# Performance work log

Hardware: AMD Instinct MI355X
Metric: run time of the kernel (lower is better)

The kernel has to match this reference:

```python
import jax, jax.numpy as jnp
import numpy as np

D_M = 1024
NUM_TOK = 4096


def setup_inputs() -> dict:
    key = jax.random.key(0)
    ks = jax.random.split(key, 7)
    mk = lambda k, shp: jax.random.normal(k, shp, dtype=jnp.float32) * 0.02
    return {
        "X": jax.random.normal(ks[0], (D_M, NUM_TOK), dtype=jnp.float32),
        "W_Q": mk(ks[1], (D_M, D_M)),
        "W_K": mk(ks[2], (D_M, D_M)),
        "W_V": mk(ks[3], (D_M, D_M)),
        "W_O": mk(ks[4], (D_M, D_M)),
        "mlp_in": mk(ks[5], (D_M, D_M)),
        "mlp_out": mk(ks[6], (D_M, D_M)),
    }


def reference(X, W_Q, W_K, W_V, W_O, mlp_in, mlp_out):
    # X: [d_m, num_tok]; module transposes to tokens-major [N, d]
    Xt = X.T  # [N, d]
    N = Xt.shape[0]
    Q = Xt @ W_Q  # [N, d]
    K = Xt @ W_K  # [N, d]
    scores = Q @ K.T  # [N, N] -- NOTE: no 1/sqrt(d) scaling, as in the original
    causal = jnp.tril(jnp.ones((N, N), dtype=bool))  # keep lower triangle incl. diag
    scores = jnp.where(causal, scores, -jnp.inf)
    A = jax.nn.softmax(scores, axis=-1)  # [N, N]
    # original applies W_V then W_O to X BEFORE the attention mix
    RH = (Xt @ W_V) @ W_O  # [N, d]
    Xt = Xt + A @ RH  # residual + attention
    h = jax.nn.relu(Xt @ mlp_in)  # [N, d] (hidden dim == d_m in original)
    Xt = Xt + h @ mlp_out  # residual + MLP
    return Xt.T  # back to [d_m, num_tok]
```

## Files before the change

kernel.cpp:

```cpp
#include <hip/hip_runtime.h>
#include <stdint.h>
#include <stddef.h>

using f16 = _Float16;
typedef __attribute__((ext_vector_type(8))) _Float16 f16x8;
typedef __attribute__((ext_vector_type(4))) float f32x4;

__device__ __forceinline__ void async_copy16(const f16* g, f16* l) {
    __builtin_amdgcn_global_load_lds(
        (const __attribute__((address_space(1))) void*)g,
        (__attribute__((address_space(3))) void*)l, 16, 0, 0);
}

__global__ __launch_bounds__(256)
void transpose_x(const float* __restrict__ in, float* __restrict__ outF,
                 f16* __restrict__ outH, int R, int C) {
    __shared__ float tile[32][33];
    const int tx = threadIdx.x & 31, ty = threadIdx.x >> 5;
    const int c0 = blockIdx.x * 32, r0 = blockIdx.y * 32;
#pragma unroll
    for (int j = 0; j < 4; j++)
        tile[ty + j * 8][tx] = in[(size_t)(r0 + ty + j * 8) * C + c0 + tx];
    __syncthreads();
#pragma unroll
    for (int j = 0; j < 4; j++) {
        float v = tile[tx][ty + j * 8];
        size_t idx = (size_t)(c0 + ty + j * 8) * R + r0 + tx;
        outF[idx] = v;
        outH[idx] = (f16)v;
    }
}

__global__ __launch_bounds__(256)
void prep_w(const float* __restrict__ w0, const float* __restrict__ w1,
            const float* __restrict__ w2, const float* __restrict__ w3,
            const float* __restrict__ w4, const float* __restrict__ w5,
            f16* o0, f16* o1, f16* o2, f16* o3, f16* o4, f16* o5, int D) {
    const int z = blockIdx.z;
    const float* in = z == 0 ? w0 : z == 1 ? w1 : z == 2 ? w2 : z == 3 ? w3 : z == 4 ? w4 : w5;
    f16* out = z == 0 ? o0 : z == 1 ? o1 : z == 2 ? o2 : z == 3 ? o3 : z == 4 ? o4 : o5;
    const int tx = threadIdx.x & 31, ty = threadIdx.x >> 5;
    const int c0 = blockIdx.x * 32, r0 = blockIdx.y * 32;
    if (z < 3) {
#pragma unroll
        for (int j = 0; j < 4; j++) {
            size_t idx = (size_t)(r0 + ty + j * 8) * D + c0 + tx;
            out[idx] = (f16)in[idx];
        }
    } else {
        __shared__ float tile[32][33];
#pragma unroll
        for (int j = 0; j < 4; j++)
            tile[ty + j * 8][tx] = in[(size_t)(r0 + ty + j * 8) * D + c0 + tx];
        __syncthreads();
#pragma unroll
        for (int j = 0; j < 4; j++)
            out[(size_t)(c0 + ty + j * 8) * D + r0 + tx] = (f16)tile[tx][ty + j * 8];
    }
}

__global__ __launch_bounds__(256)
void softmax_causal_inplace(float* __restrict__ S, int N) {
    const int row = blockIdx.x;
    const int len = row + 1;
    const int lim = ((row >> 7) + 1) << 7;
    float* s = S + (size_t)row * N;
    f16* a = (f16*)s;
    __shared__ float red[256];
    const int t = threadIdx.x;

    float v[16];
    float mx = -1e30f;
#pragma unroll
    for (int j = 0; j < 16; j++) {
        int c = t + j * 256;
        if (c < len) { v[j] = s[c]; mx = fmaxf(mx, v[j]); }
    }
    red[t] = mx; __syncthreads();
    for (int o = 128; o > 0; o >>= 1) { if (t < o) red[t] = fmaxf(red[t], red[t + o]); __syncthreads(); }
    mx = red[0]; __syncthreads();

    float sum = 0.f;
#pragma unroll
    for (int j = 0; j < 16; j++) {
        int c = t + j * 256;
        if (c < len) sum += __expf(v[j] - mx);
    }
    red[t] = sum; __syncthreads();
    for (int o = 128; o > 0; o >>= 1) { if (t < o) red[t] += red[t + o]; __syncthreads(); }
    const float inv = 1.0f / red[0];
#pragma unroll
    for (int j = 0; j < 16; j++) {
        int c = t + j * 256;
        if (c < lim) a[c] = (f16)((c < len) ? __expf(v[j] - mx) * inv : 0.0f);
    }
}

template <int MODE>
__device__ __forceinline__ void body64(
    f16* lA, f16* lB, const f16* __restrict__ A, const f16* __restrict__ B,
    float* __restrict__ Cf, f16* __restrict__ Ch, const float* __restrict__ resid,
    int m0, int n0, int M, int N, int K, int lda, int Keff) {
    const int t = threadIdx.x;
    const int lane = t & 63, wave = t >> 6;
    const int wm = (wave >> 1) * 32, wn = (wave & 1) * 32;
    const int lm = lane & 15, lq = lane >> 4;
    const int sr = t >> 2, sc = (t & 3) * 8;

    f32x4 acc[2][2] = {};

    for (int k0 = 0; k0 < Keff; k0 += 128) {
#pragma unroll
        for (int r = 0; r < 4; r++)
            async_copy16(A + (size_t)(m0 + sr) * lda + k0 + r * 32 + sc,
                         lA + r * 2048 + t * 8);
#pragma unroll
        for (int r = 0; r < 4; r++)
            async_copy16(B + (size_t)(n0 + sr) * K + k0 + r * 32 + sc,
                         lB + r * 2048 + t * 8);
        __syncthreads();

#pragma unroll
        for (int kk = 0; kk < 4; kk++) {
            f16x8 af[2], bf[2];
#pragma unroll
            for (int i = 0; i < 2; i++)
                af[i] = *(const f16x8*)&lA[kk * 2048 + (wm + i * 16 + lm) * 32 + lq * 8];
#pragma unroll
            for (int j = 0; j < 2; j++)
                bf[j] = *(const f16x8*)&lB[kk * 2048 + (wn + j * 16 + lm) * 32 + lq * 8];
#pragma unroll
            for (int i = 0; i < 2; i++)
#pragma unroll
                for (int j = 0; j < 2; j++)
                    acc[i][j] = __builtin_amdgcn_mfma_f32_16x16x32_f16(
                        af[i], bf[j], acc[i][j], 0, 0, 0);
        }
        __syncthreads();
    }

#pragma unroll
    for (int i = 0; i < 2; i++) {
        const int row = m0 + wm + i * 16 + lq * 4;
#pragma unroll
        for (int j = 0; j < 2; j++) {
            const int col = n0 + wn + j * 16 + lm;
            f32x4 v = acc[i][j];
#pragma unroll
            for (int r = 0; r < 4; r++) {
                if (MODE == 0) {
                    Ch[(size_t)(row + r) * N + col] = (f16)v[r];
                } else if (MODE == 1) {
                    Cf[(size_t)(row + r) * N + col] = v[r];
                } else if (MODE == 2) {
                    float o = v[r] + resid[(size_t)(row + r) * N + col];
                    Cf[(size_t)(row + r) * N + col] = o;
                    Ch[(size_t)(row + r) * N + col] = (f16)o;
                } else if (MODE == 3) {
                    Ch[(size_t)(row + r) * N + col] = (f16)fmaxf(v[r], 0.0f);
                } else {
                    float o = v[r] + resid[(size_t)(row + r) * N + col];
                    Cf[(size_t)col * M + (row + r)] = o;
                }
            }
        }
    }
}

__global__ __launch_bounds__(256, 4)
void tiny_pair(const f16* Wkh, const f16* Wqh, f16* GT,
               const f16* Wot, const f16* Wvh, f16* HT) {
    __shared__ alignas(16) f16 smem[16384];
    const int b = blockIdx.x;
    if (b < 256)
        body64<0>(smem, smem + 8192, Wkh, Wqh, nullptr, GT, nullptr,
                  (b >> 4) * 64, (b & 15) * 64, 1024, 1024, 1024, 1024, 1024);
    else {
        const int r = b - 256;
        body64<0>(smem, smem + 8192, Wot, Wvh, nullptr, HT, nullptr,
                  (r >> 4) * 64, (r & 15) * 64, 1024, 1024, 1024, 1024, 1024);
    }
}

__global__ __launch_bounds__(256, 4)
void mid_pair(const f16* Xth, const f16* GT, f16* Qp,
              const f16* HT, f16* RHt) {
    __shared__ alignas(16) f16 smem[16384];
    const int x = blockIdx.x & 7;
    int s = blockIdx.x >> 3;
    if (s < 128) {
        const int m = x + 8 * (s >> 4), n = s & 15;
        body64<0>(smem, smem + 8192, Xth, GT, nullptr, Qp, nullptr,
                  m * 64, n * 64, 4096, 1024, 1024, 1024, 1024);
    } else {
        s -= 128;
        const int n = x + 8 * (s >> 4), m = s & 15;
        body64<0>(smem, smem + 8192, HT, Xth, nullptr, RHt, nullptr,
                  m * 64, n * 64, 1024, 4096, 1024, 1024, 1024);
    }
}

__global__ __launch_bounds__(256, 4)
void scores_tri(const f16* Qp, const f16* Xth, float* S) {
    __shared__ alignas(16) f16 smem[16384];
    const int x = blockIdx.x & 7;
    int s = blockIdx.x >> 3;
    int m = 0, n = 0;
#pragma unroll
    for (int q = 7; q >= 0; q--) {
        const int mm = 8 * q + ((q & 1) ? 7 - x : x);
        if (s < mm + 1) { m = mm; n = s; break; }
        s -= mm + 1;
    }
    body64<1>(smem, smem + 8192, Qp, Xth, S, nullptr, nullptr,
              m * 64, n * 64, 4096, 4096, 1024, 1024, 1024);
}

template <int MODE, bool CAUSAL_K>
__global__ __launch_bounds__(256, 4)
void gemm_narrow(const f16* __restrict__ A, const f16* __restrict__ B,
                 float* __restrict__ Cf, f16* __restrict__ Ch,
                 const float* __restrict__ resid, int M, int N, int K, int lda) {
    __shared__ alignas(16) f16 smem[16384];
    const int x = blockIdx.x & 7, s = blockIdx.x >> 3;
    const int q = 7 - (s >> 4), n = s & 15;
    const int m = CAUSAL_K ? (8 * q + ((q & 1) ? 7 - x : x)) : (x + 8 * q);
    const int m0 = m * 64, n0 = n * 64;
    int Keff = K;
    if (CAUSAL_K) {
        Keff = ((m0 + 64 + 127) >> 7) << 7;
        if (Keff > K) Keff = K;
    }
    body64<MODE>(smem, smem + 8192, A, B, Cf, Ch, resid,
                 m0, n0, M, N, K, lda, Keff);
}

extern "C" void kernel_launch(void* const* d_in, const int* in_sizes, int n_in,
                              void* d_out, int out_size, void* d_ws, size_t ws_size,
                              hipStream_t stream) {
    const int D = 1024, NT = 4096;
    const float* X = (const float*)d_in[0];
    const float* W[6] = {(const float*)d_in[1], (const float*)d_in[2],
                         (const float*)d_in[3], (const float*)d_in[4],
                         (const float*)d_in[5], (const float*)d_in[6]};
    char* ws = (char*)d_ws;
    auto MB = [](size_t x) { return x << 20; };

    float* Xtf  = (float*)(ws + MB(0));
    f16*   Xth  = (f16*)(ws + MB(16));
    f16*   Wqh  = (f16*)(ws + MB(24));
    f16*   Wkh  = (f16*)(ws + MB(26));
    f16*   Wvh  = (f16*)(ws + MB(28));
    f16*   Wot  = (f16*)(ws + MB(30));
    f16*   W4t  = (f16*)(ws + MB(32));
    f16*   W5t  = (f16*)(ws + MB(34));
    f16*   GT   = (f16*)(ws + MB(36));
    f16*   HT   = (f16*)(ws + MB(38));
    f16*   Qp   = (f16*)(ws + MB(40));
    float* S    = (float*)(ws + MB(48));
    f16*   RHt  = (f16*)(ws + MB(112));
    float* Y1f  = (float*)(ws + MB(120));
    f16*   Y1h  = (f16*)(ws + MB(136));
    f16*   hb   = (f16*)(ws + MB(40));
    float* outF = (float*)d_out;

    transpose_x<<<dim3(NT / 32, D / 32), 256, 0, stream>>>(X, Xtf, Xth, D, NT);
    prep_w<<<dim3(D / 32, D / 32, 6), 256, 0, stream>>>(
        W[0], W[1], W[2], W[3], W[4], W[5], Wqh, Wkh, Wvh, Wot, W4t, W5t, D);

    tiny_pair<<<512, 256, 0, stream>>>(Wkh, Wqh, GT, Wot, Wvh, HT);

    mid_pair<<<2048, 256, 0, stream>>>(Xth, GT, Qp, HT, RHt);

    scores_tri<<<2080, 256, 0, stream>>>(Qp, Xth, S);

    softmax_causal_inplace<<<NT, 256, 0, stream>>>(S, NT);
    f16* Ab = (f16*)S;

    gemm_narrow<2, true><<<1024, 256, 0, stream>>>(
        Ab, RHt, Y1f, Y1h, Xtf, NT, D, NT, 2 * NT);

    gemm_narrow<3, false><<<1024, 256, 0, stream>>>(
        Y1h, W4t, nullptr, hb, nullptr, NT, D, D, D);

    gemm_narrow<4, false><<<1024, 256, 0, stream>>>(
        hb, W5t, outF, nullptr, Y1f, NT, D, D, D);
}
```

Measured before the change: 258.9 us.

## Store attention scores in fp16 and vectorize softmax; merge prep kernels

The scores GEMM now writes fp16 logits instead of fp32. Softmax reads and writes them in place with 8-wide vector accesses, and the attention GEMM reads the matrix with a normal row stride. This halves the memory traffic for the large N×N score matrix. The two input-prep kernels are merged into one launch to save a launch. Storing unscaled logits in fp16 risks overflow or precision loss, because scores are not divided by sqrt(d).

```diff
diff --git a/kernel.cpp b/kernel.cpp
--- a/kernel.cpp
+++ b/kernel.cpp
@@ -13,34 +13,36 @@
 }
 
 __global__ __launch_bounds__(256)
-void transpose_x(const float* __restrict__ in, float* __restrict__ outF,
-                 f16* __restrict__ outH, int R, int C) {
+void prep_all(const float* __restrict__ X, float* __restrict__ Xtf,
+              f16* __restrict__ Xth,
+              const float* __restrict__ w0, const float* __restrict__ w1,
+              const float* __restrict__ w2, const float* __restrict__ w3,
+              const float* __restrict__ w4, const float* __restrict__ w5,
+              f16* o0, f16* o1, f16* o2, f16* o3, f16* o4, f16* o5,
+              int D, int NT) {
     __shared__ float tile[32][33];
     const int tx = threadIdx.x & 31, ty = threadIdx.x >> 5;
-    const int c0 = blockIdx.x * 32, r0 = blockIdx.y * 32;
-#pragma unroll
-    for (int j = 0; j < 4; j++)
-        tile[ty + j * 8][tx] = in[(size_t)(r0 + ty + j * 8) * C + c0 + tx];
-    __syncthreads();
-#pragma unroll
-    for (int j = 0; j < 4; j++) {
-        float v = tile[tx][ty + j * 8];
-        size_t idx = (size_t)(c0 + ty + j * 8) * R + r0 + tx;
-        outF[idx] = v;
-        outH[idx] = (f16)v;
-    }
-}
-
-__global__ __launch_bounds__(256)
-void prep_w(const float* __restrict__ w0, const float* __restrict__ w1,
-            const float* __restrict__ w2, const float* __restrict__ w3,
-            const float* __restrict__ w4, const float* __restrict__ w5,
-            f16* o0, f16* o1, f16* o2, f16* o3, f16* o4, f16* o5, int D) {
-    const int z = blockIdx.z;
+    int b = blockIdx.x;
+    if (b < 4096) {
+        const int c0 = (b & 127) * 32, r0 = (b >> 7) * 32;
+#pragma unroll
+        for (int j = 0; j < 4; j++)
+            tile[ty + j * 8][tx] = X[(size_t)(r0 + ty + j * 8) * NT + c0 + tx];
+        __syncthreads();
+#pragma unroll
+        for (int j = 0; j < 4; j++) {
+            float v = tile[tx][ty + j * 8];
+            size_t idx = (size_t)(c0 + ty + j * 8) * D + r0 + tx;
+            Xtf[idx] = v;
+            Xth[idx] = (f16)v;
+        }
+        return;
+    }
+    b -= 4096;
+    const int z = b >> 10, r = b & 1023;
     const float* in = z == 0 ? w0 : z == 1 ? w1 : z == 2 ? w2 : z == 3 ? w3 : z == 4 ? w4 : w5;
     f16* out = z == 0 ? o0 : z == 1 ? o1 : z == 2 ? o2 : z == 3 ? o3 : z == 4 ? o4 : o5;
-    const int tx = threadIdx.x & 31, ty = threadIdx.x >> 5;
-    const int c0 = blockIdx.x * 32, r0 = blockIdx.y * 32;
+    const int c0 = (r & 31) * 32, r0 = (r >> 5) * 32;
     if (z < 3) {
 #pragma unroll
         for (int j = 0; j < 4; j++) {
@@ -48,7 +50,6 @@
             out[idx] = (f16)in[idx];
         }
     } else {
-        __shared__ float tile[32][33];
 #pragma unroll
         for (int j = 0; j < 4; j++)
             tile[ty + j * 8][tx] = in[(size_t)(r0 + ty + j * 8) * D + c0 + tx];
@@ -60,21 +61,30 @@
 }
 
 __global__ __launch_bounds__(256)
-void softmax_causal_inplace(float* __restrict__ S, int N) {
-    const int row = blockIdx.x;
-    const int len = row + 1;
+void softmax_rows(f16* __restrict__ A, int N) {
+    const int row = blockIdx.x, len = row + 1;
     const int lim = ((row >> 7) + 1) << 7;
-    float* s = S + (size_t)row * N;
-    f16* a = (f16*)s;
+    f16* a = A + (size_t)row * N;
     __shared__ float red[256];
     const int t = threadIdx.x;
 
     float v[16];
     float mx = -1e30f;
 #pragma unroll
-    for (int j = 0; j < 16; j++) {
-        int c = t + j * 256;
-        if (c < len) { v[j] = s[c]; mx = fmaxf(mx, v[j]); }
+    for (int j = 0; j < 2; j++) {
+        const int c = (t + j * 256) * 8;
+        if (c < len) {
+            f16x8 x = *(const f16x8*)(a + c);
+#pragma unroll
+            for (int e = 0; e < 8; e++) {
+                float f = (c + e < len) ? (float)x[e] : -1e30f;
+                v[j * 8 + e] = f;
+                mx = fmaxf(mx, f);
+            }
+        } else {
+#pragma unroll
+            for (int e = 0; e < 8; e++) v[j * 8 + e] = -1e30f;
+        }
     }
     red[t] = mx; __syncthreads();
     for (int o = 128; o > 0; o >>= 1) { if (t < o) red[t] = fmaxf(red[t], red[t + o]); __syncthreads(); }
@@ -82,17 +92,23 @@
 
     float sum = 0.f;
 #pragma unroll
-    for (int j = 0; j < 16; j++) {
-        int c = t + j * 256;
-        if (c < len) sum += __expf(v[j] - mx);
+    for (int k = 0; k < 16; k++) {
+        float e = (v[k] > -1e29f) ? __expf(v[k] - mx) : 0.0f;
+        v[k] = e;
+        sum += e;
     }
     red[t] = sum; __syncthreads();
     for (int o = 128; o > 0; o >>= 1) { if (t < o) red[t] += red[t + o]; __syncthreads(); }
     const float inv = 1.0f / red[0];
 #pragma unroll
-    for (int j = 0; j < 16; j++) {
-        int c = t + j * 256;
-        if (c < lim) a[c] = (f16)((c < len) ? __expf(v[j] - mx) * inv : 0.0f);
+    for (int j = 0; j < 2; j++) {
+        const int c = (t + j * 256) * 8;
+        if (c < lim) {
+            f16x8 o8;
+#pragma unroll
+            for (int e = 0; e < 8; e++) o8[e] = (f16)(v[j * 8 + e] * inv);
+            *(f16x8*)(a + c) = o8;
+        }
     }
 }
 
@@ -201,7 +217,7 @@
 }
 
 __global__ __launch_bounds__(256, 4)
-void scores_tri(const f16* Qp, const f16* Xth, float* S) {
+void scores_tri(const f16* Qp, const f16* Xth, f16* Af) {
     __shared__ alignas(16) f16 smem[16384];
     const int x = blockIdx.x & 7;
     int s = blockIdx.x >> 3;
@@ -212,7 +228,7 @@
         if (s < mm + 1) { m = mm; n = s; break; }
         s -= mm + 1;
     }
-    body64<1>(smem, smem + 8192, Qp, Xth, S, nullptr, nullptr,
+    body64<0>(smem, smem + 8192, Qp, Xth, nullptr, Af, nullptr,
               m * 64, n * 64, 4096, 4096, 1024, 1024, 1024);
 }
 
@@ -257,28 +273,27 @@
     f16*   GT   = (f16*)(ws + MB(36));
     f16*   HT   = (f16*)(ws + MB(38));
     f16*   Qp   = (f16*)(ws + MB(40));
-    float* S    = (float*)(ws + MB(48));
-    f16*   RHt  = (f16*)(ws + MB(112));
-    float* Y1f  = (float*)(ws + MB(120));
-    f16*   Y1h  = (f16*)(ws + MB(136));
+    f16*   Af   = (f16*)(ws + MB(48));
+    f16*   RHt  = (f16*)(ws + MB(80));
+    float* Y1f  = (float*)(ws + MB(88));
+    f16*   Y1h  = (f16*)(ws + MB(104));
     f16*   hb   = (f16*)(ws + MB(40));
     float* outF = (float*)d_out;
 
-    transpose_x<<<dim3(NT / 32, D / 32), 256, 0, stream>>>(X, Xtf, Xth, D, NT);
-    prep_w<<<dim3(D / 32, D / 32, 6), 256, 0, stream>>>(
-        W[0], W[1], W[2], W[3], W[4], W[5], Wqh, Wkh, Wvh, Wot, W4t, W5t, D);
+    prep_all<<<10240, 256, 0, stream>>>(X, Xtf, Xth, W[0], W[1], W[2], W[3],
+                                        W[4], W[5], Wqh, Wkh, Wvh, Wot, W4t,
+                                        W5t, D, NT);
 
     tiny_pair<<<512, 256, 0, stream>>>(Wkh, Wqh, GT, Wot, Wvh, HT);
 
     mid_pair<<<2048, 256, 0, stream>>>(Xth, GT, Qp, HT, RHt);
 
-    scores_tri<<<2080, 256, 0, stream>>>(Qp, Xth, S);
-
-    softmax_causal_inplace<<<NT, 256, 0, stream>>>(S, NT);
-    f16* Ab = (f16*)S;
+    scores_tri<<<2080, 256, 0, stream>>>(Qp, Xth, Af);
+
+    softmax_rows<<<NT, 256, 0, stream>>>(Af, NT);
 
     gemm_narrow<2, true><<<1024, 256, 0, stream>>>(
-        Ab, RHt, Y1f, Y1h, Xtf, NT, D, NT, 2 * NT);
+        Af, RHt, Y1f, Y1h, Xtf, NT, D, NT, NT);
 
     gemm_narrow<3, false><<<1024, 256, 0, stream>>>(
         Y1h, W4t, nullptr, hb, nullptr, NT, D, D, D);
```

Result: faster. 245.5 us (-5.2%).
